# Kernel optimization log

Hardware: AMD Instinct MI355X
Metric: run time of the kernel (lower is better)

## Reference

```python
import jax, jax.numpy as jnp
import numpy as np

EPS = 1e-12  # matches torch F.normalize default eps


def setup_inputs() -> dict:
    key = jax.random.key(0)
    ks = jax.random.split(key, 8)
    B, N, D, H = 8, 2048, 128, 128
    s = 1.0 / np.sqrt(D)
    return {
        "x": jax.random.normal(ks[0], (B, N, D), dtype=jnp.float32),
        "edge_weight": jax.random.uniform(ks[1], (B, N, N), dtype=jnp.float32),
        "W0": jax.random.normal(ks[2], (D, H), dtype=jnp.float32) * s,
        "b0": jnp.zeros((H,), dtype=jnp.float32),
        "W1": jax.random.normal(ks[3], (H, H), dtype=jnp.float32) * s,
        "b1": jnp.zeros((H,), dtype=jnp.float32),
        "W2": jax.random.normal(ks[4], (H, H), dtype=jnp.float32) * s,
        "b2": jnp.zeros((H,), dtype=jnp.float32),
    }


def _adapt_conv(h, edge_weight, W, b, is_last):
    h = h @ W + b                                   # [B,N,H]
    norm = jnp.linalg.norm(h, axis=-1, keepdims=True)
    nh = h / jnp.maximum(norm, EPS)                 # L2 normalize (F.normalize)
    cos = jnp.einsum('bij,bkj->bik', nh, nh)        # [B,N,N] cosine similarity
    ew = edge_weight * cos                          # elementwise mask
    h = jnp.einsum('bpq,bqc->bpc', ew, h)           # weighted aggregation
    if not is_last:
        h = jax.nn.relu(h)                          # dropout p=0.0 -> identity
    return h


def reference(x, edge_weight, W0, b0, W1, b1, W2, b2):
    params = [(W0, b0), (W1, b1), (W2, b2)]
    h = x
    n_layers = len(params)
    for i, (W, b) in enumerate(params):
        h = _adapt_conv(h, edge_weight, W, b, is_last=(i == n_layers - 1))
    return h
```

## Files before the change

### kernel.cpp

```cpp
#include <hip/hip_runtime.h>
#include <hip/hip_bf16.h>
#include <math.h>


typedef __attribute__((ext_vector_type(8)))  short bf16x8;
typedef __attribute__((ext_vector_type(4)))  short bf16x4;
typedef __attribute__((ext_vector_type(4)))  float f32x4;
typedef __attribute__((ext_vector_type(16))) float f32x16;

static constexpr int kB = 8, kN = 2048, kH = 128;

static __device__ __forceinline__ ushort bf16bits(float f) {
    __hip_bfloat16 hb = __float2bfloat16(f);
    return *reinterpret_cast<ushort*>(&hb);
}
static __device__ __forceinline__ unsigned pk2(float lo, float hi) {
    return (unsigned)bf16bits(lo) | ((unsigned)bf16bits(hi) << 16);
}

#define LDS_BARRIER()                                          \
    do {                                                       \
        asm volatile("s_waitcnt lgkmcnt(0)" ::: "memory");     \
        __builtin_amdgcn_s_barrier();                          \
        __builtin_amdgcn_sched_barrier(0);                     \
    } while (0)

__global__ __launch_bounds__(256) void cvt_bf16_kernel(
    const float* __restrict__ src, ushort* __restrict__ dst, int n4)
{
    int i = blockIdx.x * 256 + threadIdx.x;
    if (i >= n4) return;
    float4 v = ((const float4*)src)[i];
    bf16x4 o;
    o[0] = (short)bf16bits(v.x); o[1] = (short)bf16bits(v.y);
    o[2] = (short)bf16bits(v.z); o[3] = (short)bf16bits(v.w);
    ((bf16x4*)dst)[i] = o;
}

__global__ __launch_bounds__(256) void cvt_wT_kernel(
    const float* __restrict__ W0, const float* __restrict__ W1,
    const float* __restrict__ W2, ushort* __restrict__ WT)
{
    const float* W = blockIdx.y == 0 ? W0 : (blockIdx.y == 1 ? W1 : W2);
    int i = blockIdx.x * 256 + threadIdx.x;
    int d = i >> 7, c = i & 127;
    WT[(size_t)blockIdx.y * kH * kH + c * kH + d] = bf16bits(W[d * kH + c]);
}

__global__ __launch_bounds__(256) void linear_tr_kernel(
    const ushort* __restrict__ h16, const ushort* __restrict__ WT,
    const float* __restrict__ bias, ushort* __restrict__ t16,
    ushort* __restrict__ tT16, float* __restrict__ invn)
{
    __shared__ float ssb[64][2];
    __shared__ ushort tr[128 * 72];

    const int tid = threadIdx.x, lane = tid & 63, wid = tid >> 6;
    const int wr = wid >> 1, wc = wid & 1, quad = lane >> 4, l16 = lane & 15;
    const int rowbase = blockIdx.x * 64;
    const int b = rowbase / kN, q0 = rowbase % kN;

    f32x4 acc[2][4];
#pragma unroll
    for (int i = 0; i < 2; ++i)
#pragma unroll
        for (int ct = 0; ct < 4; ++ct) acc[i][ct] = (f32x4){0.f, 0.f, 0.f, 0.f};

#pragma unroll
    for (int k = 0; k < 4; ++k) {
        bf16x8 Af[2], Bf[4];
#pragma unroll
        for (int i = 0; i < 2; ++i)
            Af[i] = *(const bf16x8*)&h16[(size_t)(rowbase + wr * 32 + i * 16 + l16) * kH + k * 32 + quad * 8];
#pragma unroll
        for (int ct = 0; ct < 4; ++ct)
            Bf[ct] = *(const bf16x8*)&WT[(size_t)(wc * 64 + ct * 16 + l16) * kH + k * 32 + quad * 8];
#pragma unroll
        for (int i = 0; i < 2; ++i)
#pragma unroll
            for (int ct = 0; ct < 4; ++ct)
                acc[i][ct] = __builtin_amdgcn_mfma_f32_16x16x32_bf16(Af[i], Bf[ct], acc[i][ct], 0, 0, 0);
    }

    float bsr[4];
#pragma unroll
    for (int ct = 0; ct < 4; ++ct) bsr[ct] = bias[wc * 64 + ct * 16 + l16];

    f32x4 ss[2] = {(f32x4){0,0,0,0}, (f32x4){0,0,0,0}};
#pragma unroll
    for (int i = 0; i < 2; ++i)
#pragma unroll
        for (int ct = 0; ct < 4; ++ct)
#pragma unroll
            for (int r = 0; r < 4; ++r) {
                float v = acc[i][ct][r] + bsr[ct];
                acc[i][ct][r] = v;
                ss[i][r] += v * v;
            }
#pragma unroll
    for (int step = 1; step < 16; step <<= 1)
#pragma unroll
        for (int i = 0; i < 2; ++i)
#pragma unroll
            for (int r = 0; r < 4; ++r) ss[i][r] += __shfl_xor(ss[i][r], step);

    if (l16 == 0)
#pragma unroll
        for (int i = 0; i < 2; ++i)
#pragma unroll
            for (int r = 0; r < 4; ++r)
                ssb[wr * 32 + i * 16 + quad * 4 + r][wc] = ss[i][r];
    __syncthreads();
    if (tid < 64) {
        float s2 = ssb[tid][0] + ssb[tid][1];
        invn[rowbase + tid] = 1.f / fmaxf(sqrtf(s2), 1e-12f);
    }

#pragma unroll
    for (int i = 0; i < 2; ++i)
#pragma unroll
        for (int ct = 0; ct < 4; ++ct)
#pragma unroll
            for (int r = 0; r < 4; ++r) {
                const int pl = wr * 32 + i * 16 + quad * 4 + r;
                const int c = wc * 64 + ct * 16 + l16;
                ushort bits = bf16bits(acc[i][ct][r]);
                t16[(size_t)(rowbase + pl) * kH + c] = bits;
                tr[c * 72 + pl] = bits;
            }
    __syncthreads();

    ushort* tTb = tT16 + (size_t)b * kH * kN;
#pragma unroll
    for (int it = 0; it < 4; ++it) {
        int idx = tid + 256 * it;
        int c = idx >> 3, ch = idx & 7;
        bf16x8 v = *(const bf16x8*)&tr[c * 72 + ch * 8];
        *(bf16x8*)&tTb[(size_t)c * kN + q0 + ch * 8] = v;
    }
}

__global__ __launch_bounds__(512, 2) void agg_kernel(
    const ushort* __restrict__ t, const ushort* __restrict__ tT,
    const float* __restrict__ invn, const float* __restrict__ ew,
    ushort* __restrict__ hout, float* __restrict__ fout, int last)
{
    __shared__ char lds[98304];

    const int b = blockIdx.x, pbase = blockIdx.y * 64;
    const int tid = threadIdx.x, lane = tid & 63, wid = tid >> 6;
    const int wp = wid >> 2, wq = wid & 3;
    const int l31 = lane & 31, h = lane >> 5;

    const ushort* tb  = t  + (size_t)b * kN * kH;
    const ushort* tTb = tT + (size_t)b * kH * kN;
    const float*  ewb = ew + (size_t)b * kN * kN;
    const float*  invb = invn + b * kN;

    char* TQ   = lds;
    char* TT   = lds + 32768;
    char* myEw = lds + 65536 + wid * 4096;

    const int pbg = pbase + wp * 32;

    bf16x8 tP[8];
#pragma unroll
    for (int m = 0; m < 8; ++m)
        tP[m] = *(const bf16x8*)&tb[(size_t)(pbg + l31) * kH + m * 16 + h * 8];

    f32x16 oacc[4];
#pragma unroll
    for (int ct = 0; ct < 4; ++ct)
#pragma unroll
        for (int r = 0; r < 16; ++r) oacc[ct][r] = 0.f;

    const int sgRow = tid >> 4, sgCh = tid & 15;
    const int ewR = lane >> 3, ewQ = lane & 7;

    bf16x8 rQ[4], rT[4];
    f32x4 eC[4], iqC;

    auto prefetch = [&](int qb) {
#pragma unroll
        for (int j = 0; j < 4; ++j) {
            rQ[j] = *(const bf16x8*)&tb[(size_t)(qb + sgRow + 32 * j) * kH + sgCh * 8];
            rT[j] = *(const bf16x8*)&tTb[(size_t)(sgRow + 32 * j) * kN + qb + sgCh * 8];
        }
        iqC = *(const f32x4*)&invb[qb + wq * 32 + ewQ * 4];
#pragma unroll
        for (int j = 0; j < 4; ++j)
            eC[j] = *(const f32x4*)&ewb[(size_t)(pbg + 8 * j + ewR) * kN + qb + wq * 32 + ewQ * 4];
    };
    prefetch(0);

    auto buildFrags = [&](const f32x16& s, bf16x8* out2) {
        f32x4 ef[4];
#pragma unroll
        for (int g = 0; g < 4; ++g)
            ef[g] = *(const f32x4*)&myEw[l31 * 128 + ((32 * g + 16 * h) ^ ((l31 & 7) << 4))];
        float sv[16];
#pragma unroll
        for (int r = 0; r < 16; ++r) sv[r] = s[r] * ef[r >> 2][r & 3];
#pragma unroll
        for (int kk = 0; kk < 2; ++kk) {
            const int e0 = kk * 8;
            unsigned a0 = pk2(sv[e0 + 0], sv[e0 + 1]);
            unsigned a1 = pk2(sv[e0 + 2], sv[e0 + 3]);
            unsigned b0 = pk2(sv[e0 + 4], sv[e0 + 5]);
            unsigned b1 = pk2(sv[e0 + 6], sv[e0 + 7]);
            const unsigned ta0 = (unsigned)__shfl_xor((int)a0, 32);
            const unsigned ta1 = (unsigned)__shfl_xor((int)a1, 32);
            const unsigned tb0 = (unsigned)__shfl_xor((int)b0, 32);
            const unsigned tb1 = (unsigned)__shfl_xor((int)b1, 32);
            union { unsigned u[4]; bf16x8 v; } U;
            U.u[0] = h ? tb0 : a0;
            U.u[1] = h ? tb1 : a1;
            U.u[2] = h ? b0  : ta0;
            U.u[3] = h ? b1  : ta1;
            out2[kk] = U.v;
        }
    };

    for (int it = 0; it < 16; ++it) {
#pragma unroll
        for (int j = 0; j < 4; ++j) {
            const int row = sgRow + 32 * j;
            const int swz = (row & 15) << 4;
            *(bf16x8*)&TQ[row * 256 + ((sgCh * 16) ^ swz)] = rQ[j];
            *(bf16x8*)&TT[row * 256 + ((sgCh * 16) ^ swz)] = rT[j];
        }
#pragma unroll
        for (int j = 0; j < 4; ++j) {
            const int row = 8 * j + ewR;
            f32x4 e = eC[j] * iqC;
            *(f32x4*)&myEw[row * 128 + ((ewQ * 16) ^ ((row & 7) << 4))] = e;
        }
        LDS_BARRIER();

        if (it < 15) prefetch((it + 1) * 128);

        f32x16 s0;
#pragma unroll
        for (int r = 0; r < 16; ++r) s0[r] = 0.f;
        const int qrow = wq * 32 + l31;
        const int qswz = (qrow & 15) << 4;
#pragma unroll
        for (int m = 0; m < 8; ++m) {
            bf16x8 a = *(const bf16x8*)&TQ[qrow * 256 + ((m * 32 + 16 * h) ^ qswz)];
            s0 = __builtin_amdgcn_mfma_f32_32x32x16_bf16(a, tP[m], s0, 0, 0, 0);
        }

        bf16x8 aw[2];
        buildFrags(s0, aw);

#pragma unroll
        for (int kkt = 0; kkt < 2; ++kkt) {
#pragma unroll
            for (int ct = 0; ct < 4; ++ct) {
                const int crow = 32 * ct + l31;
                bf16x8 Bf = *(const bf16x8*)&TT[crow * 256 +
                              ((wq * 64 + kkt * 32 + 16 * h) ^ ((crow & 15) << 4))];
                oacc[ct] = __builtin_amdgcn_mfma_f32_32x32x16_bf16(aw[kkt], Bf, oacc[ct], 0, 0, 0);
            }
        }
        LDS_BARRIER();
    }

    __syncthreads();
    float* OL = (float*)lds;
#pragma unroll
    for (int w = 0; w < 4; ++w) {
        if (wq == w) {
#pragma unroll
            for (int ct = 0; ct < 4; ++ct)
#pragma unroll
                for (int r = 0; r < 16; ++r) {
                    const int pl = wp * 32 + (r & 3) + 8 * (r >> 2) + 4 * h;
                    const int idx = pl * 128 + 32 * ct + l31;
                    if (w == 0) OL[idx] = oacc[ct][r];
                    else        OL[idx] += oacc[ct][r];
                }
        }
        __syncthreads();
    }

    {
        const int p = tid >> 3, cb = (tid & 7) * 16;
        const float ip = invb[pbase + p];
        const size_t gbase = (size_t)b * kN * kH + (size_t)(pbase + p) * kH + cb;
        if (!last) {
#pragma unroll
            for (int u = 0; u < 2; ++u) {
                bf16x8 o;
#pragma unroll
                for (int k = 0; k < 8; ++k)
                    o[k] = (short)bf16bits(fmaxf(OL[p * 128 + cb + u * 8 + k] * ip, 0.f));
                *(bf16x8*)&hout[gbase + u * 8] = o;
            }
        } else {
#pragma unroll
            for (int u = 0; u < 4; ++u) {
                f32x4 o;
#pragma unroll
                for (int k = 0; k < 4; ++k)
                    o[k] = OL[p * 128 + cb + u * 4 + k] * ip;
                *(f32x4*)&fout[gbase + u * 4] = o;
            }
        }
    }
}

extern "C" void kernel_launch(void* const* d_in, const int* in_sizes, int n_in,
                              void* d_out, int out_size, void* d_ws, size_t ws_size,
                              hipStream_t stream) {
    const float* x  = (const float*)d_in[0];
    const float* ew = (const float*)d_in[1];
    const float* W0 = (const float*)d_in[2];
    const float* b0 = (const float*)d_in[3];
    const float* W1 = (const float*)d_in[4];
    const float* b1 = (const float*)d_in[5];
    const float* W2 = (const float*)d_in[6];
    const float* b2 = (const float*)d_in[7];
    const float* bias[3] = {b0, b1, b2};

    const size_t nBNH = (size_t)kB * kN * kH;
    ushort* h16  = (ushort*)d_ws;
    ushort* t16  = h16 + nBNH;
    ushort* tT16 = t16 + nBNH;
    float*  invn = (float*)(tT16 + nBNH);
    ushort* WT   = (ushort*)(invn + (size_t)kB * kN);
    float*  out  = (float*)d_out;

    cvt_bf16_kernel<<<(int)(nBNH / 4 + 255) / 256, 256, 0, stream>>>(x, h16, (int)(nBNH / 4));
    cvt_wT_kernel<<<dim3(64, 3), 256, 0, stream>>>(W0, W1, W2, WT);

    for (int layer = 0; layer < 3; ++layer) {
        linear_tr_kernel<<<kB * kN / 64, 256, 0, stream>>>(
            h16, WT + (size_t)layer * kH * kH, bias[layer], t16, tT16, invn);
        agg_kernel<<<dim3(kB, kN / 64), 512, 0, stream>>>(
            t16, tT16, invn, ew, h16, out, layer == 2 ? 1 : 0);
    }
}
```

Baseline: 312.6 us.

## Double-buffer agg LDS tiles, pre-normalize rows, store edge weights as bf16

The linear kernel now writes L2-normalized rows directly, so the separate inverse-norm buffer and its per-tile loads and scaling in the aggregation kernel go away. The aggregation kernel double-buffers the Q/T tiles in LDS, issues the next prefetch before the barrier and drops one barrier per iteration. Edge weights are staged in LDS as bf16, halving that footprint. The score MFMA chain is split across two accumulators to shorten dependencies. LDS grows to 144KB per block, which limits residency to one block per CU, and bf16 edge weights add rounding error.

```diff
diff --git a/kernel.cpp b/kernel.cpp
--- a/kernel.cpp
+++ b/kernel.cpp
@@ -7,6 +7,7 @@
 typedef __attribute__((ext_vector_type(4)))  short bf16x4;
 typedef __attribute__((ext_vector_type(4)))  float f32x4;
 typedef __attribute__((ext_vector_type(16))) float f32x16;
+typedef __attribute__((ext_vector_type(2)))  unsigned u32x2;
 
 static constexpr int kB = 8, kN = 2048, kH = 128;
 
@@ -16,6 +17,12 @@
 }
 static __device__ __forceinline__ unsigned pk2(float lo, float hi) {
     return (unsigned)bf16bits(lo) | ((unsigned)bf16bits(hi) << 16);
+}
+static __device__ __forceinline__ float bf2f_lo(unsigned u) {
+    unsigned v = u << 16; float f; __builtin_memcpy(&f, &v, 4); return f;
+}
+static __device__ __forceinline__ float bf2f_hi(unsigned u) {
+    unsigned v = u & 0xffff0000u; float f; __builtin_memcpy(&f, &v, 4); return f;
 }
 
 #define LDS_BARRIER()                                          \
@@ -49,8 +56,8 @@
 
 __global__ __launch_bounds__(256) void linear_tr_kernel(
     const ushort* __restrict__ h16, const ushort* __restrict__ WT,
-    const float* __restrict__ bias, ushort* __restrict__ t16,
-    ushort* __restrict__ tT16, float* __restrict__ invn)
+    const float* __restrict__ bias, ushort* __restrict__ tn16,
+    ushort* __restrict__ tT16)
 {
     __shared__ float ssb[64][2];
     __shared__ ushort tr[128 * 72];
@@ -111,10 +118,16 @@
             for (int r = 0; r < 4; ++r)
                 ssb[wr * 32 + i * 16 + quad * 4 + r][wc] = ss[i][r];
     __syncthreads();
-    if (tid < 64) {
-        float s2 = ssb[tid][0] + ssb[tid][1];
-        invn[rowbase + tid] = 1.f / fmaxf(sqrtf(s2), 1e-12f);
-    }
+
+    float invr[2][4];
+#pragma unroll
+    for (int i = 0; i < 2; ++i)
+#pragma unroll
+        for (int r = 0; r < 4; ++r) {
+            const int pl = wr * 32 + i * 16 + quad * 4 + r;
+            float s2 = ssb[pl][0] + ssb[pl][1];
+            invr[i][r] = 1.f / fmaxf(sqrtf(s2), 1e-12f);
+        }
 
 #pragma unroll
     for (int i = 0; i < 2; ++i)
@@ -124,9 +137,9 @@
             for (int r = 0; r < 4; ++r) {
                 const int pl = wr * 32 + i * 16 + quad * 4 + r;
                 const int c = wc * 64 + ct * 16 + l16;
-                ushort bits = bf16bits(acc[i][ct][r]);
-                t16[(size_t)(rowbase + pl) * kH + c] = bits;
-                tr[c * 72 + pl] = bits;
+                const float v = acc[i][ct][r];
+                tn16[(size_t)(rowbase + pl) * kH + c] = bf16bits(v * invr[i][r]);
+                tr[c * 72 + pl] = bf16bits(v);
             }
     __syncthreads();
 
@@ -141,25 +154,24 @@
 }
 
 __global__ __launch_bounds__(512, 2) void agg_kernel(
-    const ushort* __restrict__ t, const ushort* __restrict__ tT,
-    const float* __restrict__ invn, const float* __restrict__ ew,
+    const ushort* __restrict__ tn, const ushort* __restrict__ tT,
+    const float* __restrict__ ew,
     ushort* __restrict__ hout, float* __restrict__ fout, int last)
 {
-    __shared__ char lds[98304];
+    __shared__ char lds[147456];
 
     const int b = blockIdx.x, pbase = blockIdx.y * 64;
     const int tid = threadIdx.x, lane = tid & 63, wid = tid >> 6;
     const int wp = wid >> 2, wq = wid & 3;
     const int l31 = lane & 31, h = lane >> 5;
 
-    const ushort* tb  = t  + (size_t)b * kN * kH;
+    const ushort* tb  = tn + (size_t)b * kN * kH;
     const ushort* tTb = tT + (size_t)b * kH * kN;
     const float*  ewb = ew + (size_t)b * kN * kN;
-    const float*  invb = invn + b * kN;
 
     char* TQ   = lds;
-    char* TT   = lds + 32768;
-    char* myEw = lds + 65536 + wid * 4096;
+    char* TT   = lds + 65536;
+    char* myEw = lds + 131072 + wid * 2048;
 
     const int pbg = pbase + wp * 32;
 
@@ -178,7 +190,7 @@
     const int ewR = lane >> 3, ewQ = lane & 7;
 
     bf16x8 rQ[4], rT[4];
-    f32x4 eC[4], iqC;
+    f32x4 eC[4];
 
     auto prefetch = [&](int qb) {
 #pragma unroll
@@ -186,21 +198,22 @@
             rQ[j] = *(const bf16x8*)&tb[(size_t)(qb + sgRow + 32 * j) * kH + sgCh * 8];
             rT[j] = *(const bf16x8*)&tTb[(size_t)(sgRow + 32 * j) * kN + qb + sgCh * 8];
         }
-        iqC = *(const f32x4*)&invb[qb + wq * 32 + ewQ * 4];
 #pragma unroll
         for (int j = 0; j < 4; ++j)
             eC[j] = *(const f32x4*)&ewb[(size_t)(pbg + 8 * j + ewR) * kN + qb + wq * 32 + ewQ * 4];
     };
     prefetch(0);
 
-    auto buildFrags = [&](const f32x16& s, bf16x8* out2) {
-        f32x4 ef[4];
-#pragma unroll
-        for (int g = 0; g < 4; ++g)
-            ef[g] = *(const f32x4*)&myEw[l31 * 128 + ((32 * g + 16 * h) ^ ((l31 & 7) << 4))];
+    auto buildFrags = [&](const f32x16& sa, const f32x16& sb, bf16x8* out2) {
         float sv[16];
 #pragma unroll
-        for (int r = 0; r < 16; ++r) sv[r] = s[r] * ef[r >> 2][r & 3];
+        for (int g = 0; g < 4; ++g) {
+            u32x2 ev = *(const u32x2*)&myEw[l31 * 64 + ((16 * g + 8 * h) ^ ((l31 & 7) << 3))];
+            sv[4 * g + 0] = (sa[4 * g + 0] + sb[4 * g + 0]) * bf2f_lo(ev[0]);
+            sv[4 * g + 1] = (sa[4 * g + 1] + sb[4 * g + 1]) * bf2f_hi(ev[0]);
+            sv[4 * g + 2] = (sa[4 * g + 2] + sb[4 * g + 2]) * bf2f_lo(ev[1]);
+            sv[4 * g + 3] = (sa[4 * g + 3] + sb[4 * g + 3]) * bf2f_hi(ev[1]);
+        }
 #pragma unroll
         for (int kk = 0; kk < 2; ++kk) {
             const int e0 = kk * 8;
@@ -222,48 +235,53 @@
     };
 
     for (int it = 0; it < 16; ++it) {
+        const int sBase = (it & 1) * 32768;
+
 #pragma unroll
         for (int j = 0; j < 4; ++j) {
             const int row = sgRow + 32 * j;
             const int swz = (row & 15) << 4;
-            *(bf16x8*)&TQ[row * 256 + ((sgCh * 16) ^ swz)] = rQ[j];
-            *(bf16x8*)&TT[row * 256 + ((sgCh * 16) ^ swz)] = rT[j];
+            *(bf16x8*)&TQ[sBase + row * 256 + ((sgCh * 16) ^ swz)] = rQ[j];
+            *(bf16x8*)&TT[sBase + row * 256 + ((sgCh * 16) ^ swz)] = rT[j];
         }
 #pragma unroll
         for (int j = 0; j < 4; ++j) {
             const int row = 8 * j + ewR;
-            f32x4 e = eC[j] * iqC;
-            *(f32x4*)&myEw[row * 128 + ((ewQ * 16) ^ ((row & 7) << 4))] = e;
-        }
+            u32x2 w;
+            w[0] = pk2(eC[j][0], eC[j][1]);
+            w[1] = pk2(eC[j][2], eC[j][3]);
+            *(u32x2*)&myEw[row * 64 + ((ewQ * 8) ^ ((row & 7) << 3))] = w;
+        }
+
+        if (it < 15) prefetch((it + 1) * 128);
+
         LDS_BARRIER();
 
-        if (it < 15) prefetch((it + 1) * 128);
-
-        f32x16 s0;
-#pragma unroll
-        for (int r = 0; r < 16; ++r) s0[r] = 0.f;
+        f32x16 s0a, s0b;
+#pragma unroll
+        for (int r = 0; r < 16; ++r) { s0a[r] = 0.f; s0b[r] = 0.f; }
         const int qrow = wq * 32 + l31;
         const int qswz = (qrow & 15) << 4;
 #pragma unroll
         for (int m = 0; m < 8; ++m) {
-            bf16x8 a = *(const bf16x8*)&TQ[qrow * 256 + ((m * 32 + 16 * h) ^ qswz)];
-            s0 = __builtin_amdgcn_mfma_f32_32x32x16_bf16(a, tP[m], s0, 0, 0, 0);
+            bf16x8 a = *(const bf16x8*)&TQ[sBase + qrow * 256 + ((m * 32 + 16 * h) ^ qswz)];
+            if (m & 1) s0b = __builtin_amdgcn_mfma_f32_32x32x16_bf16(a, tP[m], s0b, 0, 0, 0);
+            else       s0a = __builtin_amdgcn_mfma_f32_32x32x16_bf16(a, tP[m], s0a, 0, 0, 0);
         }
 
         bf16x8 aw[2];
-        buildFrags(s0, aw);
+        buildFrags(s0a, s0b, aw);
 
 #pragma unroll
         for (int kkt = 0; kkt < 2; ++kkt) {
 #pragma unroll
             for (int ct = 0; ct < 4; ++ct) {
                 const int crow = 32 * ct + l31;
-                bf16x8 Bf = *(const bf16x8*)&TT[crow * 256 +
+                bf16x8 Bf = *(const bf16x8*)&TT[sBase + crow * 256 +
                               ((wq * 64 + kkt * 32 + 16 * h) ^ ((crow & 15) << 4))];
                 oacc[ct] = __builtin_amdgcn_mfma_f32_32x32x16_bf16(aw[kkt], Bf, oacc[ct], 0, 0, 0);
             }
         }
-        LDS_BARRIER();
     }
 
     __syncthreads();
@@ -286,7 +304,6 @@
 
     {
         const int p = tid >> 3, cb = (tid & 7) * 16;
-        const float ip = invb[pbase + p];
         const size_t gbase = (size_t)b * kN * kH + (size_t)(pbase + p) * kH + cb;
         if (!last) {
 #pragma unroll
@@ -294,7 +311,7 @@
                 bf16x8 o;
 #pragma unroll
                 for (int k = 0; k < 8; ++k)
-                    o[k] = (short)bf16bits(fmaxf(OL[p * 128 + cb + u * 8 + k] * ip, 0.f));
+                    o[k] = (short)bf16bits(fmaxf(OL[p * 128 + cb + u * 8 + k], 0.f));
                 *(bf16x8*)&hout[gbase + u * 8] = o;
             }
         } else {
@@ -303,7 +320,7 @@
                 f32x4 o;
 #pragma unroll
                 for (int k = 0; k < 4; ++k)
-                    o[k] = OL[p * 128 + cb + u * 4 + k] * ip;
+                    o[k] = OL[p * 128 + cb + u * 4 + k];
                 *(f32x4*)&fout[gbase + u * 4] = o;
             }
         }
@@ -325,10 +342,9 @@
 
     const size_t nBNH = (size_t)kB * kN * kH;
     ushort* h16  = (ushort*)d_ws;
-    ushort* t16  = h16 + nBNH;
-    ushort* tT16 = t16 + nBNH;
-    float*  invn = (float*)(tT16 + nBNH);
-    ushort* WT   = (ushort*)(invn + (size_t)kB * kN);
+    ushort* tn16 = h16 + nBNH;
+    ushort* tT16 = tn16 + nBNH;
+    ushort* WT   = tT16 + nBNH;
     float*  out  = (float*)d_out;
 
     cvt_bf16_kernel<<<(int)(nBNH / 4 + 255) / 256, 256, 0, stream>>>(x, h16, (int)(nBNH / 4));
@@ -336,8 +352,8 @@
 
     for (int layer = 0; layer < 3; ++layer) {
         linear_tr_kernel<<<kB * kN / 64, 256, 0, stream>>>(
-            h16, WT + (size_t)layer * kH * kH, bias[layer], t16, tT16, invn);
+            h16, WT + (size_t)layer * kH * kH, bias[layer], tn16, tT16);
         agg_kernel<<<dim3(kB, kN / 64), 512, 0, stream>>>(
-            t16, tT16, invn, ew, h16, out, layer == 2 ? 1 : 0);
-    }
-}
+            tn16, tT16, ew, h16, out, layer == 2 ? 1 : 0);
+    }
+}
```

New measurement: 314.7 us. No clear change (+0.6%).
